# Performance work log

Measured on AMD Instinct MI355X. Metric: run time of the kernel, lower is better.

Reference implementation:

```python
import jax, jax.numpy as jnp
import numpy as np

N = 100000   # nodes
E = 1600000  # edges
G = 64       # graphs in batch
H, C = 8, 16 # heads, per-head channels
HID = H * C  # 128
EMB, BBOX, TOK, REL = 256, 32, 151, 51
IN0 = EMB + BBOX  # 288
NEG_SLOPE = 0.2
BN_EPS = 1e-5


def setup_inputs() -> dict:
    key = jax.random.key(0)
    ks = jax.random.split(key, 32)
    f = lambda i, shape: jax.random.normal(ks[i], shape, dtype=jnp.float32) * 0.05
    inp = {}
    inp["tok_id"] = jax.random.randint(ks[0], (N,), 0, TOK)
    inp["bbox"] = jax.random.normal(ks[1], (N, 4), dtype=jnp.float32)
    inp["edge_index"] = jax.random.randint(ks[2], (2, E), 0, N)
    inp["edge_attr"] = jax.random.randint(ks[3], (E,), 0, REL)
    inp["batch"] = jnp.sort(jax.random.randint(ks[4], (N,), 0, G))
    inp["tok_emb"] = f(5, (TOK, EMB))
    inp["bbox_W"] = f(6, (4, BBOX)); inp["bbox_b"] = f(7, (BBOX,))
    inp["rel_emb"] = f(8, (REL, C))
    # layer 0 (in_dim 288 -> 128)
    inp["Wl0"] = f(9, (IN0, HID));  inp["bl0"] = f(10, (HID,))
    inp["Wr0"] = f(11, (IN0, HID)); inp["br0"] = f(12, (HID,))
    inp["We0"] = f(13, (C, HID));   inp["att0"] = f(14, (H, C))
    inp["bias0"] = f(15, (HID,))
    inp["gamma0"] = jnp.ones((HID,), jnp.float32); inp["beta0"] = jnp.zeros((HID,), jnp.float32)
    # layers 1..2 stacked (128 -> 128)
    inp["WlS"] = f(16, (2, HID, HID)); inp["blS"] = f(17, (2, HID))
    inp["WrS"] = f(18, (2, HID, HID)); inp["brS"] = f(19, (2, HID))
    inp["WeS"] = f(20, (2, C, HID));   inp["attS"] = f(21, (2, H, C))
    inp["biasS"] = f(22, (2, HID))
    inp["gammaS"] = jnp.ones((2, HID), jnp.float32); inp["betaS"] = jnp.zeros((2, HID), jnp.float32)
    return inp


def gatv2_layer(x, src, dst, e_emb, Wl, bl, Wr, br, We, att, bias):
    """GATv2Conv: gather -> leaky_relu attention -> segment softmax -> scatter."""
    xl = (x @ Wl + bl).reshape(-1, H, C)   # source transform [N,H,C]
    xr = (x @ Wr + br).reshape(-1, H, C)   # target transform [N,H,C]
    ee = (e_emb @ We).reshape(-1, H, C)    # edge transform  [E,H,C]
    m = jax.nn.leaky_relu(xl[src] + xr[dst] + ee, NEG_SLOPE)  # [E,H,C]
    logits = jnp.einsum('ehc,hc->eh', m, att)                 # [E,H]
    amax = jax.ops.segment_max(logits, dst, num_segments=N)   # [N,H]
    p = jnp.exp(logits - amax[dst])
    denom = jax.ops.segment_sum(p, dst, num_segments=N)       # [N,H]
    alpha = p / jnp.maximum(denom[dst], 1e-16)                # [E,H]
    out = jax.ops.segment_sum(alpha[..., None] * xl[src], dst, num_segments=N)  # [N,H,C]
    return out.reshape(-1, HID) + bias


def batch_norm(x, gamma, beta):
    mu = jnp.mean(x, axis=0)
    var = jnp.var(x, axis=0)
    return gamma * (x - mu) * jax.lax.rsqrt(var + BN_EPS) + beta


def reference(tok_id, bbox, edge_index, edge_attr, batch,
              tok_emb, bbox_W, bbox_b, rel_emb,
              Wl0, bl0, Wr0, br0, We0, att0, bias0, gamma0, beta0,
              WlS, blS, WrS, brS, WeS, attS, biasS, gammaS, betaS):
    src, dst = edge_index[0], edge_index[1]
    x = jnp.concatenate([tok_emb[tok_id], bbox @ bbox_W + bbox_b], axis=-1)  # [N,288]
    e_emb = rel_emb[edge_attr]  # [E,16]
    h = batch_norm(jax.nn.relu(
        gatv2_layer(x, src, dst, e_emb, Wl0, bl0, Wr0, br0, We0, att0, bias0)),
        gamma0, beta0)
    for i in range(2):
        h = h + batch_norm(jax.nn.relu(
            gatv2_layer(h, src, dst, e_emb, WlS[i], blS[i], WrS[i], brS[i], WeS[i], attS[i], biasS[i])),
            gammaS[i], betaS[i])
    # global mean pool over graphs
    sums = jax.ops.segment_sum(h, batch, num_segments=G)
    counts = jax.ops.segment_sum(jnp.ones((h.shape[0],), h.dtype), batch, num_segments=G)
    return sums / jnp.maximum(counts, 1.0)[:, None]  # [G,128]
```

## Files before the change

### kernel.cpp

```cpp
#include <hip/hip_runtime.h>

#define N_NODES 100000
#define N_PAD   100096
#define N_EDGES 1600000
#define NGRAPH  64
#define NHEAD   8
#define NCH     16
#define HID     128
#define IN0     288
#define NREL    51
#define EMB     256
#define NBBOX   32
#define NEG_SLOPE 0.2f
#define EPS_BN  1e-5f
#define AGG_BLOCKS 2048
#define POOL_BLOCKS 1024
#define SENT 0x03F00000u
#define SENT_MIN ((uint)(NREL) << 20)
#define L2E 1.4426950408889634f

typedef unsigned int uint;
typedef unsigned short ushort;

typedef __bf16 bf16_t;
typedef bf16_t bfx8 __attribute__((ext_vector_type(8)));
typedef float  fx4  __attribute__((ext_vector_type(4)));
typedef float  v2f  __attribute__((ext_vector_type(2)));

__device__ __forceinline__ ushort f2bf(float f) {
  uint u = __float_as_uint(f);
  u += 0x7fffu + ((u >> 16) & 1u);
  return (ushort)(u >> 16);
}
__device__ __forceinline__ float bf2f(uint u) { return __uint_as_float(u << 16); }
__device__ __forceinline__ v2f up2(uint u) {
  v2f r;
  r.x = __uint_as_float(u << 16);
  r.y = __uint_as_float(u & 0xffff0000u);
  return r;
}
__device__ __forceinline__ void unpack8(uint4 u, float* f) {
  f[0] = __uint_as_float(u.x << 16); f[1] = __uint_as_float(u.x & 0xffff0000u);
  f[2] = __uint_as_float(u.y << 16); f[3] = __uint_as_float(u.y & 0xffff0000u);
  f[4] = __uint_as_float(u.z << 16); f[5] = __uint_as_float(u.z & 0xffff0000u);
  f[6] = __uint_as_float(u.w << 16); f[7] = __uint_as_float(u.w & 0xffff0000u);
}

__global__ void se_prep(const float* __restrict__ Wl0, const float* __restrict__ Wr0,
                        const float* __restrict__ WlS, const float* __restrict__ WrS,
                        const float* __restrict__ rel_emb, const float* __restrict__ We0,
                        const float* __restrict__ WeS,
                        const float* __restrict__ bl0, const float* __restrict__ br0,
                        const float* __restrict__ blS, const float* __restrict__ brS,
                        ushort* __restrict__ W0T, ushort* __restrict__ WST,
                        float* __restrict__ eetab, float* __restrict__ biascat) {
  int i = blockIdx.x * 256 + threadIdx.x;
  if (i < 256 * IN0) {
    int j = i / IN0, k = i - j * IN0;
    float v = (j < 128) ? Wl0[k * 128 + j] : Wr0[k * 128 + (j - 128)];
    W0T[j * IN0 + k] = f2bf(v);
    return;
  }
  i -= 256 * IN0;
  if (i < 2 * 256 * HID) {
    int li = i >> 15;
    int rem = i & 32767;
    int j = rem >> 7, k = rem & 127;
    float v = (j < 128) ? WlS[(li * 128 + k) * 128 + j] : WrS[(li * 128 + k) * 128 + (j - 128)];
    WST[(li * 256 + j) * 128 + k] = f2bf(v);
    return;
  }
  i -= 2 * 256 * HID;
  if (i < 3 * NREL * HID) {
    int li = i / (NREL * HID);
    int rem = i - li * (NREL * HID);
    int r = rem >> 7, j = rem & 127;
    const float* We = (li == 0) ? We0 : (WeS + (li - 1) * NCH * HID);
    float s = 0.f;
#pragma unroll
    for (int c = 0; c < NCH; c++) s += rel_emb[r * NCH + c] * We[c * HID + j];
    eetab[li * (NREL * HID) + rem] = s;
    return;
  }
  i -= 3 * NREL * HID;
  if (i < 3 * 256) {
    int li = i >> 8, j = i & 255;
    const float* bl = (li == 0) ? bl0 : (blS + (li - 1) * HID);
    const float* br = (li == 0) ? br0 : (brS + (li - 1) * HID);
    biascat[i] = (j < 128) ? bl[j] : br[j - 128];
  }
}

__global__ void se_build_x(const int* __restrict__ tok_id, const float* __restrict__ bbox,
                           const float* __restrict__ tok_emb, const float* __restrict__ bbox_W,
                           const float* __restrict__ bbox_b, ushort* __restrict__ x) {
  int idx = blockIdx.x * 256 + threadIdx.x;
  if (idx >= N_PAD * 36) return;
  int n = idx / 36, c = (idx - n * 36) * 8;
  float f[8];
  if (n >= N_NODES) {
#pragma unroll
    for (int j = 0; j < 8; j++) f[j] = 0.f;
  } else if (c < EMB) {
    const float* te = tok_emb + (size_t)tok_id[n] * EMB + c;
    const float4 t0 = *(const float4*)te, t1 = *(const float4*)(te + 4);
    f[0] = t0.x; f[1] = t0.y; f[2] = t0.z; f[3] = t0.w;
    f[4] = t1.x; f[5] = t1.y; f[6] = t1.z; f[7] = t1.w;
  } else {
    const int j0 = c - EMB;
    const float4 bb = *(const float4*)(bbox + (size_t)n * 4);
#pragma unroll
    for (int j = 0; j < 8; j++) {
      float v = bbox_b[j0 + j];
      v += bb.x * bbox_W[0 * NBBOX + j0 + j];
      v += bb.y * bbox_W[1 * NBBOX + j0 + j];
      v += bb.z * bbox_W[2 * NBBOX + j0 + j];
      v += bb.w * bbox_W[3 * NBBOX + j0 + j];
      f[j] = v;
    }
  }
  uint4 p;
  p.x = ((uint)f2bf(f[1]) << 16) | f2bf(f[0]);
  p.y = ((uint)f2bf(f[3]) << 16) | f2bf(f[2]);
  p.z = ((uint)f2bf(f[5]) << 16) | f2bf(f[4]);
  p.w = ((uint)f2bf(f[7]) << 16) | f2bf(f[6]);
  ((uint4*)x)[idx] = p;
}

__global__ void se_hist(const int* __restrict__ ei, int* __restrict__ deg) {
  int e = blockIdx.x * 256 + threadIdx.x;
  if (e < N_EDGES) atomicAdd(&deg[ei[N_EDGES + e]], 1);
}
__global__ __launch_bounds__(1024) void se_scanA(const int* __restrict__ deg,
                                                 int* __restrict__ offs, int* __restrict__ bsum) {
  __shared__ int s[1024];
  const int tid = threadIdx.x;
  const int i = blockIdx.x * 1024 + tid;
  int v = (i < N_NODES) ? ((deg[i] + 3) & ~3) : 0;
  s[tid] = v;
  __syncthreads();
  for (int d = 1; d < 1024; d <<= 1) {
    int t = (tid >= d) ? s[tid - d] : 0;
    __syncthreads();
    s[tid] += t;
    __syncthreads();
  }
  if (i < N_NODES) offs[i] = s[tid] - v;
  if (tid == 1023) bsum[blockIdx.x] = s[1023];
}
__global__ __launch_bounds__(128) void se_scanB(int* __restrict__ bsum, int nb) {
  __shared__ int s[128];
  const int t = threadIdx.x;
  int v = (t < nb) ? bsum[t] : 0;
  s[t] = v;
  __syncthreads();
  for (int d = 1; d < 128; d <<= 1) {
    int u = (t >= d) ? s[t - d] : 0;
    __syncthreads();
    s[t] += u;
    __syncthreads();
  }
  if (t < nb) bsum[t] = s[t] - v;
}
__global__ __launch_bounds__(1024) void se_scanC(int* __restrict__ offs, const int* __restrict__ bsum) {
  int i = blockIdx.x * 1024 + threadIdx.x;
  if (i < N_NODES) offs[i] += bsum[blockIdx.x];
}
__global__ void se_padfill(const int* __restrict__ deg, const int* __restrict__ offs,
                           uint* __restrict__ csrp, int2* __restrict__ rowinfo) {
  int n = blockIdx.x * 256 + threadIdx.x;
  if (n >= N_NODES) return;
  const int d = deg[n];
  const int o = offs[n];
  rowinfo[n] = make_int2(o, (d + 3) >> 2);
  const int s = o + d;
  const int c = ((d + 3) & ~3) - d;
  for (int j = 0; j < c; j++) csrp[s + j] = SENT;
  if (n == N_NODES - 1) {
    const int e = o + ((d + 3) & ~3);
    for (int j = 0; j < 64; j++) csrp[e + j] = SENT;
  }
}
__global__ void se_scatter(const int* __restrict__ ei, const int* __restrict__ eattr,
                           const int* __restrict__ offs, int* __restrict__ cur,
                           uint* __restrict__ csrp) {
  int e = blockIdx.x * 256 + threadIdx.x;
  if (e < N_EDGES) {
    int d = ei[N_EDGES + e];
    int p = offs[d] + atomicAdd(&cur[d], 1);
    csrp[p] = (uint)ei[e] | ((uint)eattr[e] << 20);
  }
}

template <int K>
__global__ __launch_bounds__(256) void se_gemm(const ushort* __restrict__ A,
                                               const ushort* __restrict__ BT,
                                               const float* __restrict__ bias,
                                               ushort* __restrict__ C) {
  __shared__ __align__(16) ushort As[128 * 32];
  __shared__ __align__(16) ushort Bs[128 * 32];
  const int tid = threadIdx.x;
  const int w = tid >> 6, l = tid & 63;
  const int wr = w >> 1, wc = w & 1;
  const int m0 = blockIdx.x * 128, n0 = blockIdx.y * 128;
  fx4 acc[4][4];
#pragma unroll
  for (int i = 0; i < 4; i++)
#pragma unroll
    for (int j = 0; j < 4; j++) acc[i][j] = fx4{0.f, 0.f, 0.f, 0.f};

  for (int k0 = 0; k0 < K; k0 += 32) {
#pragma unroll
    for (int ch = 0; ch < 2; ch++) {
      const int t = tid + ch * 256;
      const int r = t >> 2, c = (t & 3) << 3;
      const ushort* ga = A + (size_t)(m0 + r) * K + (k0 + c);
      ushort* la = As + (size_t)(ch * 256 + w * 64) * 8;
      __builtin_amdgcn_global_load_lds((const __attribute__((address_space(1))) void*)ga,
                                       (__attribute__((address_space(3))) void*)la, 16, 0, 0);
      const ushort* gb = BT + (size_t)(n0 + r) * K + (k0 + c);
      ushort* lb = Bs + (size_t)(ch * 256 + w * 64) * 8;
      __builtin_amdgcn_global_load_lds((const __attribute__((address_space(1))) void*)gb,
                                       (__attribute__((address_space(3))) void*)lb, 16, 0, 0);
    }
    __syncthreads();
    bfx8 af[4], bfr[4];
#pragma unroll
    for (int i = 0; i < 4; i++) {
      af[i]  = *(const bfx8*)(As + ((wr * 64 + i * 16 + (l & 15)) * 32 + ((l >> 4) * 8)));
      bfr[i] = *(const bfx8*)(Bs + ((wc * 64 + i * 16 + (l & 15)) * 32 + ((l >> 4) * 8)));
    }
#pragma unroll
    for (int i = 0; i < 4; i++)
#pragma unroll
      for (int j = 0; j < 4; j++)
        acc[i][j] = __builtin_amdgcn_mfma_f32_16x16x32_bf16(af[i], bfr[j], acc[i][j], 0, 0, 0);
    __syncthreads();
  }
#pragma unroll
  for (int i = 0; i < 4; i++) {
    const int rbase = m0 + wr * 64 + i * 16 + ((l >> 4) << 2);
#pragma unroll
    for (int j = 0; j < 4; j++) {
      const int col = n0 + wc * 64 + j * 16 + (l & 15);
      const float bz = bias[col];
#pragma unroll
      for (int r2 = 0; r2 < 4; r2++) {
        const int row = rbase + r2;
        if (row < N_NODES) C[(size_t)row * 256 + col] = f2bf(acc[i][j][r2] + bz);
      }
    }
  }
}

__global__ __launch_bounds__(256) void se_agg(const uint4* __restrict__ xlxr4,
                                              const uint* __restrict__ csrp,
                                              const int2* __restrict__ rowinfo,
                                              const float* __restrict__ eetab,
                                              const float* __restrict__ att,
                                              const float* __restrict__ bias,
                                              float* __restrict__ y, float* __restrict__ partial) {
  __shared__ ushort ee[64 * HID];
  __shared__ float bstat[256];
  const int tid = threadIdx.x, w = tid >> 6, l = tid & 63;
  const int g = l >> 4, k = l & 15;
  for (int i = tid; i < 64 * HID; i += 256) {
    const int r = i >> 7;
    ee[i] = (r < NREL) ? f2bf(eetab[i]) : (ushort)0;
  }
  bstat[tid] = 0.f;
  __syncthreads();
  v2f a1v[4], a2v[4];
  {
    const float* ap = att + (k >> 1) * NCH + (k & 1) * 8;
#pragma unroll
    for (int q = 0; q < 4; q++) {
      a1v[q] = v2f{ap[2 * q] * (0.6f * L2E), ap[2 * q + 1] * (0.6f * L2E)};
      a2v[q] = v2f{ap[2 * q] * (0.4f * L2E), ap[2 * q + 1] * (0.4f * L2E)};
    }
  }
  v2f sv[4], qv[4];
#pragma unroll
  for (int q = 0; q < 4; q++) { sv[q] = v2f{0.f, 0.f}; qv[q] = v2f{0.f, 0.f}; }
  const v2f zero = v2f{0.f, 0.f};

  const int stride = gridDim.x * 4;
  for (int n = blockIdx.x * 4 + w; n < N_NODES; n += stride) {
    const int2 ri = rowinfo[n];
    const uint* rowp = csrp + ri.x + g;
    const int nit = ri.y;
    v2f xrv[4];
    {
      const uint4 xru = xlxr4[(uint)n * 32u + 16u + (uint)k];
      xrv[0] = up2(xru.x); xrv[1] = up2(xru.y); xrv[2] = up2(xru.z); xrv[3] = up2(xru.w);
    }
    float den = 0.f;
    v2f acc[4];
#pragma unroll
    for (int q = 0; q < 4; q++) acc[q] = zero;

    uint e0 = rowp[0], e1 = rowp[4], e2 = rowp[8];
    uint4 x0 = xlxr4[(e0 & 0xFFFFFu) * 32u + (uint)k];
    uint4 x1 = xlxr4[(e1 & 0xFFFFFu) * 32u + (uint)k];
    uint4 x2 = xlxr4[(e2 & 0xFFFFFu) * 32u + (uint)k];
    for (int i = 0; i < nit; ++i) {
      const uint e3 = rowp[4 * i + 12];
      const uint4 eeu = *(const uint4*)(ee + (e0 >> 20) * HID + k * 8);
      v2f sd1 = zero, sd2 = zero;
      v2f xls[4];
      {
        const uint xcu[4] = {x0.x, x0.y, x0.z, x0.w};
        const uint eu[4] = {eeu.x, eeu.y, eeu.z, eeu.w};
#pragma unroll
        for (int q = 0; q < 4; q++) {
          const v2f xl = up2(xcu[q]);
          const v2f m = xl + xrv[q] + up2(eu[q]);
          sd1 += m * a1v[q];
          sd2 += __builtin_elementwise_abs(m) * a2v[q];
          xls[q] = xl;
        }
      }
      float s = sd1.x + sd1.y + sd2.x + sd2.y;
      s += __shfl_xor(s, 1);
      s = (e0 >= SENT_MIN) ? -1e30f : s;
      const float p = exp2f(s);
      den += p;
      const v2f pp = v2f{p, p};
#pragma unroll
      for (int q = 0; q < 4; q++) acc[q] += pp * xls[q];
      e0 = e1; x0 = x1; e1 = e2; x1 = x2; e2 = e3;
      x2 = xlxr4[(e2 & 0xFFFFFu) * 32u + (uint)k];
    }
    den += __shfl_xor(den, 16);
    den += __shfl_xor(den, 32);
#pragma unroll
    for (int q = 0; q < 4; q++) {
      acc[q].x += __shfl_xor(acc[q].x, 16); acc[q].x += __shfl_xor(acc[q].x, 32);
      acc[q].y += __shfl_xor(acc[q].y, 16); acc[q].y += __shfl_xor(acc[q].y, 32);
    }
    if (g == 0) {
      const float r = 1.f / fmaxf(den, 1e-16f);
      const v2f rr = v2f{r, r};
      const float4 b0 = ((const float4*)bias)[k * 2];
      const float4 b1 = ((const float4*)bias)[k * 2 + 1];
      const v2f bv[4] = {v2f{b0.x, b0.y}, v2f{b0.z, b0.w}, v2f{b1.x, b1.y}, v2f{b1.z, b1.w}};
      v2f ov[4];
#pragma unroll
      for (int q = 0; q < 4; q++) {
        ov[q] = __builtin_elementwise_max(acc[q] * rr + bv[q], zero);
        sv[q] += ov[q];
        qv[q] += ov[q] * ov[q];
      }
      float4* yp = (float4*)y + (size_t)n * 32 + (size_t)k * 2;
      yp[0] = make_float4(ov[0].x, ov[0].y, ov[1].x, ov[1].y);
      yp[1] = make_float4(ov[2].x, ov[2].y, ov[3].x, ov[3].y);
    }
  }
  if (l < 16) {
#pragma unroll
    for (int q = 0; q < 4; q++) {
      unsafeAtomicAdd(&bstat[k * 8 + 2 * q], sv[q].x);
      unsafeAtomicAdd(&bstat[k * 8 + 2 * q + 1], sv[q].y);
      unsafeAtomicAdd(&bstat[128 + k * 8 + 2 * q], qv[q].x);
      unsafeAtomicAdd(&bstat[128 + k * 8 + 2 * q + 1], qv[q].y);
    }
  }
  __syncthreads();
  partial[(size_t)tid * AGG_BLOCKS + blockIdx.x] = bstat[tid];
}

__global__ __launch_bounds__(256) void se_stats(const float* __restrict__ partial, float* __restrict__ musig) {
  __shared__ float red[256];
  const int ch = blockIdx.x, tid = threadIdx.x;
  float s = 0.f;
  for (int i = tid; i < AGG_BLOCKS; i += 256) s += partial[ch * AGG_BLOCKS + i];
  red[tid] = s; __syncthreads();
  for (int o = 128; o > 0; o >>= 1) { if (tid < o) red[tid] += red[tid + o]; __syncthreads(); }
  const float sum = red[0]; __syncthreads();
  float q = 0.f;
  for (int i = tid; i < AGG_BLOCKS; i += 256) q += partial[(128 + ch) * AGG_BLOCKS + i];
  red[tid] = q; __syncthreads();
  for (int o = 128; o > 0; o >>= 1) { if (tid < o) red[tid] += red[tid + o]; __syncthreads(); }
  if (tid == 0) {
    const float mean = sum / (float)N_NODES;
    const float var = red[0] / (float)N_NODES - mean * mean;
    musig[ch] = mean;
    musig[128 + ch] = rsqrtf(var + EPS_BN);
  }
}

__global__ void se_bn(const float* __restrict__ y, const float* __restrict__ musig,
                      const float* __restrict__ gamma, const float* __restrict__ beta,
                      ushort* __restrict__ h_bf, int residual) {
  int idx = blockIdx.x * 256 + threadIdx.x;
  if (idx >= N_NODES * 16) return;
  const int k = idx & 15;
  const float4 y0 = ((const float4*)y)[(size_t)idx * 2];
  const float4 y1 = ((const float4*)y)[(size_t)idx * 2 + 1];
  const float4 mu0 = ((const float4*)musig)[k * 2],         mu1 = ((const float4*)musig)[k * 2 + 1];
  const float4 rs0 = ((const float4*)(musig + 128))[k * 2], rs1 = ((const float4*)(musig + 128))[k * 2 + 1];
  const float4 g0  = ((const float4*)gamma)[k * 2],         g1  = ((const float4*)gamma)[k * 2 + 1];
  const float4 b0  = ((const float4*)beta)[k * 2],          b1  = ((const float4*)beta)[k * 2 + 1];
  float v[8];
  v[0] = g0.x * (y0.x - mu0.x) * rs0.x + b0.x;
  v[1] = g0.y * (y0.y - mu0.y) * rs0.y + b0.y;
  v[2] = g0.z * (y0.z - mu0.z) * rs0.z + b0.z;
  v[3] = g0.w * (y0.w - mu0.w) * rs0.w + b0.w;
  v[4] = g1.x * (y1.x - mu1.x) * rs1.x + b1.x;
  v[5] = g1.y * (y1.y - mu1.y) * rs1.y + b1.y;
  v[6] = g1.z * (y1.z - mu1.z) * rs1.z + b1.z;
  v[7] = g1.w * (y1.w - mu1.w) * rs1.w + b1.w;
  if (residual) {
    const uint4 ho = ((const uint4*)h_bf)[idx];
    float f[8];
    unpack8(ho, f);
#pragma unroll
    for (int j = 0; j < 8; j++) v[j] += f[j];
  }
  uint4 p4;
  p4.x = ((uint)f2bf(v[1]) << 16) | f2bf(v[0]);
  p4.y = ((uint)f2bf(v[3]) << 16) | f2bf(v[2]);
  p4.z = ((uint)f2bf(v[5]) << 16) | f2bf(v[4]);
  p4.w = ((uint)f2bf(v[7]) << 16) | f2bf(v[6]);
  ((uint4*)h_bf)[idx] = p4;
}

__global__ __launch_bounds__(256) void se_pool(const ushort* __restrict__ h_bf,
                                               const int* __restrict__ batch,
                                               float* __restrict__ pool) {
  const int tid = threadIdx.x, w = tid >> 6, l = tid & 63;
  const int wid = blockIdx.x * 4 + w;
  const int nw = gridDim.x * 4;
  const int chunk = (N_NODES + nw - 1) / nw;
  const int start = wid * chunk;
  const int end = min(N_NODES, start + chunk);
  float a0 = 0.f, a1 = 0.f;
  int cg = -1, cnt = 0;
  for (int n = start; n < end; ++n) {
    const int gg = batch[n];
    if (gg != cg) {
      if (cg >= 0) {
        unsafeAtomicAdd(&pool[cg * HID + 2 * l], a0);
        unsafeAtomicAdd(&pool[cg * HID + 2 * l + 1], a1);
        if (l == 0) unsafeAtomicAdd(&pool[NGRAPH * HID + cg], (float)cnt);
      }
      a0 = 0.f; a1 = 0.f; cnt = 0; cg = gg;
    }
    const uint u = ((const uint*)h_bf)[(size_t)n * 64 + l];
    a0 += bf2f(u & 0xffffu);
    a1 += __uint_as_float(u & 0xffff0000u);
    cnt++;
  }
  if (cg >= 0) {
    unsafeAtomicAdd(&pool[cg * HID + 2 * l], a0);
    unsafeAtomicAdd(&pool[cg * HID + 2 * l + 1], a1);
    if (l == 0) unsafeAtomicAdd(&pool[NGRAPH * HID + cg], (float)cnt);
  }
}
__global__ void se_poolfin(const float* __restrict__ pool, float* __restrict__ out) {
  int idx = blockIdx.x * 256 + threadIdx.x;
  if (idx < NGRAPH * HID) {
    int g = idx >> 7;
    out[idx] = pool[idx] / fmaxf(pool[NGRAPH * HID + g], 1.f);
  }
}

extern "C" void kernel_launch(void* const* d_in, const int* in_sizes, int n_in,
                              void* d_out, int out_size, void* d_ws, size_t ws_size,
                              hipStream_t stream) {
  (void)in_sizes; (void)n_in; (void)out_size; (void)ws_size;
  const int*   tok_id  = (const int*)d_in[0];
  const float* bbox    = (const float*)d_in[1];
  const int*   ei      = (const int*)d_in[2];
  const int*   eattr   = (const int*)d_in[3];
  const int*   batch   = (const int*)d_in[4];
  const float* tok_emb = (const float*)d_in[5];
  const float* bbox_W  = (const float*)d_in[6];
  const float* bbox_b  = (const float*)d_in[7];
  const float* rel_emb = (const float*)d_in[8];
  const float* Wl0  = (const float*)d_in[9];
  const float* bl0  = (const float*)d_in[10];
  const float* Wr0  = (const float*)d_in[11];
  const float* br0  = (const float*)d_in[12];
  const float* We0  = (const float*)d_in[13];
  const float* att0 = (const float*)d_in[14];
  const float* bias0  = (const float*)d_in[15];
  const float* gamma0 = (const float*)d_in[16];
  const float* beta0  = (const float*)d_in[17];
  const float* WlS  = (const float*)d_in[18];
  const float* blS  = (const float*)d_in[19];
  const float* WrS  = (const float*)d_in[20];
  const float* brS  = (const float*)d_in[21];
  const float* WeS  = (const float*)d_in[22];
  const float* attS = (const float*)d_in[23];
  const float* biasS  = (const float*)d_in[24];
  const float* gammaS = (const float*)d_in[25];
  const float* betaS  = (const float*)d_in[26];
  float* out = (float*)d_out;

  char* ws = (char*)d_ws;
  size_t off = 0;
  auto alloc = [&](size_t bytes) -> char* {
    char* p = ws + off;
    off = (off + bytes + 255) & ~(size_t)255;
    return p;
  };
  ushort* x_bf = (ushort*)alloc((size_t)N_PAD * IN0 * 2);
  float*  y    = (float*)x_bf;
  ushort* xlxr = (ushort*)alloc((size_t)N_PAD * 256 * 2);
  ushort* h_bf = (ushort*)alloc((size_t)N_PAD * HID * 2);
  ushort* W0T  = (ushort*)alloc((size_t)256 * IN0 * 2);
  ushort* WST  = (ushort*)alloc((size_t)2 * 256 * HID * 2);
  float*  eetab   = (float*)alloc((size_t)3 * NREL * HID * 4);
  float*  biascat = (float*)alloc((size_t)3 * 256 * 4);
  int* deg  = (int*)alloc((size_t)N_NODES * 4);
  int* offs = (int*)alloc((size_t)(N_NODES + 1) * 4);
  int* cur  = (int*)alloc((size_t)N_NODES * 4);
  int* bsum = (int*)alloc(128 * 4);
  int2* rowinfo = (int2*)alloc((size_t)N_NODES * 8);
  uint* csrp = (uint*)alloc((size_t)(N_EDGES + 3 * N_NODES + 256) * 4);
  float* partial = (float*)alloc((size_t)256 * AGG_BLOCKS * 4);
  float* musig   = (float*)alloc(256 * 4);
  float* pool    = (float*)alloc((size_t)(NGRAPH * HID + NGRAPH) * 4);

  hipMemsetAsync(deg, 0, (size_t)N_NODES * 4, stream);
  hipMemsetAsync(cur, 0, (size_t)N_NODES * 4, stream);
  hipMemsetAsync(pool, 0, (size_t)(NGRAPH * HID + NGRAPH) * 4, stream);

  se_prep<<<624, 256, 0, stream>>>(Wl0, Wr0, WlS, WrS, rel_emb, We0, WeS,
                                   bl0, br0, blS, brS, W0T, WST, eetab, biascat);
  se_build_x<<<(N_PAD * 36 + 255) / 256, 256, 0, stream>>>(tok_id, bbox, tok_emb, bbox_W, bbox_b, x_bf);
  se_hist<<<(N_EDGES + 255) / 256, 256, 0, stream>>>(ei, deg);
  se_scanA<<<98, 1024, 0, stream>>>(deg, offs, bsum);
  se_scanB<<<1, 128, 0, stream>>>(bsum, 98);
  se_scanC<<<98, 1024, 0, stream>>>(offs, bsum);
  se_padfill<<<(N_NODES + 255) / 256, 256, 0, stream>>>(deg, offs, csrp, rowinfo);
  se_scatter<<<(N_EDGES + 255) / 256, 256, 0, stream>>>(ei, eattr, offs, cur, csrp);

  se_gemm<IN0><<<dim3(N_PAD / 128, 2), 256, 0, stream>>>(x_bf, W0T, biascat, xlxr);
  se_agg<<<AGG_BLOCKS, 256, 0, stream>>>((const uint4*)xlxr, csrp, rowinfo,
                                         eetab, att0, bias0, y, partial);
  se_stats<<<128, 256, 0, stream>>>(partial, musig);
  se_bn<<<(N_NODES * 16 + 255) / 256, 256, 0, stream>>>(y, musig, gamma0, beta0, h_bf, 0);

  for (int li = 0; li < 2; ++li) {
    se_gemm<HID><<<dim3(N_PAD / 128, 2), 256, 0, stream>>>(h_bf, WST + (size_t)li * 256 * HID,
                                                           biascat + (li + 1) * 256, xlxr);
    se_agg<<<AGG_BLOCKS, 256, 0, stream>>>((const uint4*)xlxr, csrp, rowinfo,
                                           eetab + (size_t)(li + 1) * NREL * HID,
                                           attS + (size_t)li * NHEAD * NCH,
                                           biasS + (size_t)li * HID, y, partial);
    se_stats<<<128, 256, 0, stream>>>(partial, musig);
    se_bn<<<(N_NODES * 16 + 255) / 256, 256, 0, stream>>>(y, musig, gammaS + (size_t)li * HID,
                                                          betaS + (size_t)li * HID, h_bf, 1);
  }

  se_pool<<<POOL_BLOCKS, 256, 0, stream>>>(h_bf, batch, pool);
  se_poolfin<<<32, 256, 0, stream>>>(pool, out);
}
```

Before: 966.2 us.

## Fold layer-0 input transform into token/bbox lookup tables; store agg output in bf16

Layer 0's GEMM over the concatenated token embedding and bbox features is replaced algebraically. A per-token table (tok_emb·W), a 4x256 bbox projection and a constant vector are precomputed in the prep kernel, and a new per-node kernel assembles xl/xr from them, removing the x build and the 288-wide GEMM. The aggregation output y is now written as bf16 instead of fp32, halving its write and BN read traffic at some precision cost. The edge prefetch pipeline in the aggregation kernel changes from a 3-deep unconditional lookahead to a bounds-guarded 1-2 deep one.

```diff
diff --git a/kernel.cpp b/kernel.cpp
--- a/kernel.cpp
+++ b/kernel.cpp
@@ -11,6 +11,7 @@
 #define NREL    51
 #define EMB     256
 #define NBBOX   32
+#define NTOK    151
 #define NEG_SLOPE 0.2f
 #define EPS_BN  1e-5f
 #define AGG_BLOCKS 2048
@@ -46,23 +47,30 @@
   f[6] = __uint_as_float(u.w << 16); f[7] = __uint_as_float(u.w & 0xffff0000u);
 }
 
+__device__ __forceinline__ float w0cat(const float* Wl0, const float* Wr0, int c, int j) {
+  return (j < 128) ? Wl0[c * 128 + j] : Wr0[c * 128 + (j - 128)];
+}
+
+#define S0 (2 * 256 * HID)
+#define S1 (3 * NREL * HID)
+#define S2 (3 * 256)
+#define S3 (NTOK * 256)
+#define S4 (4 * 256)
+#define S5 (256)
+#define PREP_TOT (S0 + S1 + S2 + S3 + S4 + S5)
 __global__ void se_prep(const float* __restrict__ Wl0, const float* __restrict__ Wr0,
                         const float* __restrict__ WlS, const float* __restrict__ WrS,
                         const float* __restrict__ rel_emb, const float* __restrict__ We0,
                         const float* __restrict__ WeS,
                         const float* __restrict__ bl0, const float* __restrict__ br0,
                         const float* __restrict__ blS, const float* __restrict__ brS,
-                        ushort* __restrict__ W0T, ushort* __restrict__ WST,
-                        float* __restrict__ eetab, float* __restrict__ biascat) {
+                        const float* __restrict__ tok_emb, const float* __restrict__ bbox_W,
+                        const float* __restrict__ bbox_b,
+                        ushort* __restrict__ WST, float* __restrict__ eetab,
+                        float* __restrict__ biascat,
+                        float* __restrict__ T, float* __restrict__ F, float* __restrict__ cvec) {
   int i = blockIdx.x * 256 + threadIdx.x;
-  if (i < 256 * IN0) {
-    int j = i / IN0, k = i - j * IN0;
-    float v = (j < 128) ? Wl0[k * 128 + j] : Wr0[k * 128 + (j - 128)];
-    W0T[j * IN0 + k] = f2bf(v);
-    return;
-  }
-  i -= 256 * IN0;
-  if (i < 2 * 256 * HID) {
+  if (i < S0) {
     int li = i >> 15;
     int rem = i & 32767;
     int j = rem >> 7, k = rem & 127;
@@ -70,8 +78,8 @@
     WST[(li * 256 + j) * 128 + k] = f2bf(v);
     return;
   }
-  i -= 2 * 256 * HID;
-  if (i < 3 * NREL * HID) {
+  i -= S0;
+  if (i < S1) {
     int li = i / (NREL * HID);
     int rem = i - li * (NREL * HID);
     int r = rem >> 7, j = rem & 127;
@@ -82,49 +90,70 @@
     eetab[li * (NREL * HID) + rem] = s;
     return;
   }
-  i -= 3 * NREL * HID;
-  if (i < 3 * 256) {
+  i -= S1;
+  if (i < S2) {
     int li = i >> 8, j = i & 255;
     const float* bl = (li == 0) ? bl0 : (blS + (li - 1) * HID);
     const float* br = (li == 0) ? br0 : (brS + (li - 1) * HID);
     biascat[i] = (j < 128) ? bl[j] : br[j - 128];
-  }
-}
-
-__global__ void se_build_x(const int* __restrict__ tok_id, const float* __restrict__ bbox,
-                           const float* __restrict__ tok_emb, const float* __restrict__ bbox_W,
-                           const float* __restrict__ bbox_b, ushort* __restrict__ x) {
+    return;
+  }
+  i -= S2;
+  if (i < S3) {
+    int t = i >> 8, j = i & 255;
+    float s = 0.f;
+    for (int c = 0; c < EMB; c++) s += tok_emb[t * EMB + c] * w0cat(Wl0, Wr0, c, j);
+    T[i] = s;
+    return;
+  }
+  i -= S3;
+  if (i < S4) {
+    int r = i >> 8, j = i & 255;
+    float s = 0.f;
+#pragma unroll
+    for (int b = 0; b < NBBOX; b++) s += bbox_W[r * NBBOX + b] * w0cat(Wl0, Wr0, EMB + b, j);
+    F[i] = s;
+    return;
+  }
+  i -= S4;
+  if (i < S5) {
+    int j = i;
+    float s = (j < 128) ? bl0[j] : br0[j - 128];
+#pragma unroll
+    for (int b = 0; b < NBBOX; b++) s += bbox_b[b] * w0cat(Wl0, Wr0, EMB + b, j);
+    cvec[j] = s;
+  }
+}
+
+__global__ void se_xform0(const int* __restrict__ tok_id, const float* __restrict__ bbox,
+                          const float* __restrict__ T, const float* __restrict__ F,
+                          const float* __restrict__ cvec, ushort* __restrict__ xlxr) {
   int idx = blockIdx.x * 256 + threadIdx.x;
-  if (idx >= N_PAD * 36) return;
-  int n = idx / 36, c = (idx - n * 36) * 8;
-  float f[8];
-  if (n >= N_NODES) {
-#pragma unroll
-    for (int j = 0; j < 8; j++) f[j] = 0.f;
-  } else if (c < EMB) {
-    const float* te = tok_emb + (size_t)tok_id[n] * EMB + c;
-    const float4 t0 = *(const float4*)te, t1 = *(const float4*)(te + 4);
-    f[0] = t0.x; f[1] = t0.y; f[2] = t0.z; f[3] = t0.w;
-    f[4] = t1.x; f[5] = t1.y; f[6] = t1.z; f[7] = t1.w;
-  } else {
-    const int j0 = c - EMB;
-    const float4 bb = *(const float4*)(bbox + (size_t)n * 4);
-#pragma unroll
-    for (int j = 0; j < 8; j++) {
-      float v = bbox_b[j0 + j];
-      v += bb.x * bbox_W[0 * NBBOX + j0 + j];
-      v += bb.y * bbox_W[1 * NBBOX + j0 + j];
-      v += bb.z * bbox_W[2 * NBBOX + j0 + j];
-      v += bb.w * bbox_W[3 * NBBOX + j0 + j];
-      f[j] = v;
-    }
+  if (idx >= N_NODES * 32) return;
+  const int n = idx >> 5, k = idx & 31;
+  const int j0 = k * 8;
+  const int t = tok_id[n];
+  const float4 bb = *(const float4*)(bbox + (size_t)n * 4);
+  float o[8];
+#pragma unroll
+  for (int h = 0; h < 2; h++) {
+    const float4 tv = *(const float4*)(T + t * 256 + j0 + 4 * h);
+    const float4 cv = *(const float4*)(cvec + j0 + 4 * h);
+    const float4 f0 = *(const float4*)(F + 0 * 256 + j0 + 4 * h);
+    const float4 f1 = *(const float4*)(F + 1 * 256 + j0 + 4 * h);
+    const float4 f2 = *(const float4*)(F + 2 * 256 + j0 + 4 * h);
+    const float4 f3 = *(const float4*)(F + 3 * 256 + j0 + 4 * h);
+    o[4 * h + 0] = tv.x + cv.x + bb.x * f0.x + bb.y * f1.x + bb.z * f2.x + bb.w * f3.x;
+    o[4 * h + 1] = tv.y + cv.y + bb.x * f0.y + bb.y * f1.y + bb.z * f2.y + bb.w * f3.y;
+    o[4 * h + 2] = tv.z + cv.z + bb.x * f0.z + bb.y * f1.z + bb.z * f2.z + bb.w * f3.z;
+    o[4 * h + 3] = tv.w + cv.w + bb.x * f0.w + bb.y * f1.w + bb.z * f2.w + bb.w * f3.w;
   }
   uint4 p;
-  p.x = ((uint)f2bf(f[1]) << 16) | f2bf(f[0]);
-  p.y = ((uint)f2bf(f[3]) << 16) | f2bf(f[2]);
-  p.z = ((uint)f2bf(f[5]) << 16) | f2bf(f[4]);
-  p.w = ((uint)f2bf(f[7]) << 16) | f2bf(f[6]);
-  ((uint4*)x)[idx] = p;
+  p.x = ((uint)f2bf(o[1]) << 16) | f2bf(o[0]);
+  p.y = ((uint)f2bf(o[3]) << 16) | f2bf(o[2]);
+  p.z = ((uint)f2bf(o[5]) << 16) | f2bf(o[4]);
+  p.w = ((uint)f2bf(o[7]) << 16) | f2bf(o[6]);
+  ((uint4*)xlxr)[idx] = p;
 }
 
 __global__ void se_hist(const int* __restrict__ ei, int* __restrict__ deg) {
@@ -259,7 +288,7 @@
                                               const float* __restrict__ eetab,
                                               const float* __restrict__ att,
                                               const float* __restrict__ bias,
-                                              float* __restrict__ y, float* __restrict__ partial) {
+                                              ushort* __restrict__ y, float* __restrict__ partial) {
   __shared__ ushort ee[64 * HID];
   __shared__ float bstat[256];
   const int tid = threadIdx.x, w = tid >> 6, l = tid & 63;
@@ -299,17 +328,24 @@
 #pragma unroll
     for (int q = 0; q < 4; q++) acc[q] = zero;
 
-    uint e0 = rowp[0], e1 = rowp[4], e2 = rowp[8];
-    uint4 x0 = xlxr4[(e0 & 0xFFFFFu) * 32u + (uint)k];
-    uint4 x1 = xlxr4[(e1 & 0xFFFFFu) * 32u + (uint)k];
-    uint4 x2 = xlxr4[(e2 & 0xFFFFFu) * 32u + (uint)k];
+    uint eA = SENT, eB = SENT;
+    uint4 xlv = uint4{0u, 0u, 0u, 0u};
+    if (nit > 0) {
+      eA = rowp[0];
+      xlv = xlxr4[(eA & 0xFFFFFu) * 32u + (uint)k];
+      if (nit > 1) eB = rowp[4];
+    }
     for (int i = 0; i < nit; ++i) {
-      const uint e3 = rowp[4 * i + 12];
-      const uint4 eeu = *(const uint4*)(ee + (e0 >> 20) * HID + k * 8);
+      const uint ec = eA;
+      const uint4 xc = xlv;
+      eA = eB;
+      if (i + 1 < nit) xlv = xlxr4[(eA & 0xFFFFFu) * 32u + (uint)k];
+      if (i + 2 < nit) eB = rowp[4 * (i + 2)];
+      const uint4 eeu = *(const uint4*)(ee + (ec >> 20) * HID + k * 8);
       v2f sd1 = zero, sd2 = zero;
       v2f xls[4];
       {
-        const uint xcu[4] = {x0.x, x0.y, x0.z, x0.w};
+        const uint xcu[4] = {xc.x, xc.y, xc.z, xc.w};
         const uint eu[4] = {eeu.x, eeu.y, eeu.z, eeu.w};
 #pragma unroll
         for (int q = 0; q < 4; q++) {
@@ -322,14 +358,12 @@
       }
       float s = sd1.x + sd1.y + sd2.x + sd2.y;
       s += __shfl_xor(s, 1);
-      s = (e0 >= SENT_MIN) ? -1e30f : s;
+      s = (ec >= SENT_MIN) ? -1e30f : s;
       const float p = exp2f(s);
       den += p;
       const v2f pp = v2f{p, p};
 #pragma unroll
       for (int q = 0; q < 4; q++) acc[q] += pp * xls[q];
-      e0 = e1; x0 = x1; e1 = e2; x1 = x2; e2 = e3;
-      x2 = xlxr4[(e2 & 0xFFFFFu) * 32u + (uint)k];
     }
     den += __shfl_xor(den, 16);
     den += __shfl_xor(den, 32);
@@ -351,9 +385,12 @@
         sv[q] += ov[q];
         qv[q] += ov[q] * ov[q];
       }
-      float4* yp = (float4*)y + (size_t)n * 32 + (size_t)k * 2;
-      yp[0] = make_float4(ov[0].x, ov[0].y, ov[1].x, ov[1].y);
-      yp[1] = make_float4(ov[2].x, ov[2].y, ov[3].x, ov[3].y);
+      uint4 p4;
+      p4.x = ((uint)f2bf(ov[0].y) << 16) | f2bf(ov[0].x);
+      p4.y = ((uint)f2bf(ov[1].y) << 16) | f2bf(ov[1].x);
+      p4.z = ((uint)f2bf(ov[2].y) << 16) | f2bf(ov[2].x);
+      p4.w = ((uint)f2bf(ov[3].y) << 16) | f2bf(ov[3].x);
+      ((uint4*)y)[(size_t)n * 16 + k] = p4;
     }
   }
   if (l < 16) {
@@ -389,33 +426,34 @@
   }
 }
 
-__global__ void se_bn(const float* __restrict__ y, const float* __restrict__ musig,
+__global__ void se_bn(const ushort* __restrict__ y, const float* __restrict__ musig,
                       const float* __restrict__ gamma, const float* __restrict__ beta,
                       ushort* __restrict__ h_bf, int residual) {
   int idx = blockIdx.x * 256 + threadIdx.x;
   if (idx >= N_NODES * 16) return;
   const int k = idx & 15;
-  const float4 y0 = ((const float4*)y)[(size_t)idx * 2];
-  const float4 y1 = ((const float4*)y)[(size_t)idx * 2 + 1];
+  const uint4 yv = ((const uint4*)y)[idx];
+  float f[8];
+  unpack8(yv, f);
   const float4 mu0 = ((const float4*)musig)[k * 2],         mu1 = ((const float4*)musig)[k * 2 + 1];
   const float4 rs0 = ((const float4*)(musig + 128))[k * 2], rs1 = ((const float4*)(musig + 128))[k * 2 + 1];
   const float4 g0  = ((const float4*)gamma)[k * 2],         g1  = ((const float4*)gamma)[k * 2 + 1];
   const float4 b0  = ((const float4*)beta)[k * 2],          b1  = ((const float4*)beta)[k * 2 + 1];
   float v[8];
-  v[0] = g0.x * (y0.x - mu0.x) * rs0.x + b0.x;
-  v[1] = g0.y * (y0.y - mu0.y) * rs0.y + b0.y;
-  v[2] = g0.z * (y0.z - mu0.z) * rs0.z + b0.z;
-  v[3] = g0.w * (y0.w - mu0.w) * rs0.w + b0.w;
-  v[4] = g1.x * (y1.x - mu1.x) * rs1.x + b1.x;
-  v[5] = g1.y * (y1.y - mu1.y) * rs1.y + b1.y;
-  v[6] = g1.z * (y1.z - mu1.z) * rs1.z + b1.z;
-  v[7] = g1.w * (y1.w - mu1.w) * rs1.w + b1.w;
+  v[0] = g0.x * (f[0] - mu0.x) * rs0.x + b0.x;
+  v[1] = g0.y * (f[1] - mu0.y) * rs0.y + b0.y;
+  v[2] = g0.z * (f[2] - mu0.z) * rs0.z + b0.z;
+  v[3] = g0.w * (f[3] - mu0.w) * rs0.w + b0.w;
+  v[4] = g1.x * (f[4] - mu1.x) * rs1.x + b1.x;
+  v[5] = g1.y * (f[5] - mu1.y) * rs1.y + b1.y;
+  v[6] = g1.z * (f[6] - mu1.z) * rs1.z + b1.z;
+  v[7] = g1.w * (f[7] - mu1.w) * rs1.w + b1.w;
   if (residual) {
     const uint4 ho = ((const uint4*)h_bf)[idx];
-    float f[8];
-    unpack8(ho, f);
-#pragma unroll
-    for (int j = 0; j < 8; j++) v[j] += f[j];
+    float fr[8];
+    unpack8(ho, fr);
+#pragma unroll
+    for (int j = 0; j < 8; j++) v[j] += fr[j];
   }
   uint4 p4;
   p4.x = ((uint)f2bf(v[1]) << 16) | f2bf(v[0]);
@@ -505,14 +543,15 @@
     off = (off + bytes + 255) & ~(size_t)255;
     return p;
   };
-  ushort* x_bf = (ushort*)alloc((size_t)N_PAD * IN0 * 2);
-  float*  y    = (float*)x_bf;
   ushort* xlxr = (ushort*)alloc((size_t)N_PAD * 256 * 2);
+  ushort* y    = (ushort*)alloc((size_t)N_NODES * HID * 2);
   ushort* h_bf = (ushort*)alloc((size_t)N_PAD * HID * 2);
-  ushort* W0T  = (ushort*)alloc((size_t)256 * IN0 * 2);
   ushort* WST  = (ushort*)alloc((size_t)2 * 256 * HID * 2);
   float*  eetab   = (float*)alloc((size_t)3 * NREL * HID * 4);
   float*  biascat = (float*)alloc((size_t)3 * 256 * 4);
+  float*  T    = (float*)alloc((size_t)NTOK * 256 * 4);
+  float*  F    = (float*)alloc((size_t)4 * 256 * 4);
+  float*  cvec = (float*)alloc((size_t)256 * 4);
   int* deg  = (int*)alloc((size_t)N_NODES * 4);
   int* offs = (int*)alloc((size_t)(N_NODES + 1) * 4);
   int* cur  = (int*)alloc((size_t)N_NODES * 4);
@@ -527,9 +566,9 @@
   hipMemsetAsync(cur, 0, (size_t)N_NODES * 4, stream);
   hipMemsetAsync(pool, 0, (size_t)(NGRAPH * HID + NGRAPH) * 4, stream);
 
-  se_prep<<<624, 256, 0, stream>>>(Wl0, Wr0, WlS, WrS, rel_emb, We0, WeS,
-                                   bl0, br0, blS, brS, W0T, WST, eetab, biascat);
-  se_build_x<<<(N_PAD * 36 + 255) / 256, 256, 0, stream>>>(tok_id, bbox, tok_emb, bbox_W, bbox_b, x_bf);
+  se_prep<<<(PREP_TOT + 255) / 256, 256, 0, stream>>>(
+      Wl0, Wr0, WlS, WrS, rel_emb, We0, WeS, bl0, br0, blS, brS,
+      tok_emb, bbox_W, bbox_b, WST, eetab, biascat, T, F, cvec);
   se_hist<<<(N_EDGES + 255) / 256, 256, 0, stream>>>(ei, deg);
   se_scanA<<<98, 1024, 0, stream>>>(deg, offs, bsum);
   se_scanB<<<1, 128, 0, stream>>>(bsum, 98);
@@ -537,7 +576,7 @@
   se_padfill<<<(N_NODES + 255) / 256, 256, 0, stream>>>(deg, offs, csrp, rowinfo);
   se_scatter<<<(N_EDGES + 255) / 256, 256, 0, stream>>>(ei, eattr, offs, cur, csrp);
 
-  se_gemm<IN0><<<dim3(N_PAD / 128, 2), 256, 0, stream>>>(x_bf, W0T, biascat, xlxr);
+  se_xform0<<<(N_NODES * 32 + 255) / 256, 256, 0, stream>>>(tok_id, bbox, T, F, cvec, xlxr);
   se_agg<<<AGG_BLOCKS, 256, 0, stream>>>((const uint4*)xlxr, csrp, rowinfo,
                                          eetab, att0, bias0, y, partial);
   se_stats<<<128, 256, 0, stream>>>(partial, musig);
```

Result: faster. 828.2 us (-14.3%).
